# Optimization experiments

Hardware: AMD Instinct MI355X
Metric: run time of the kernel (lower is better)

## Reference

```python
import jax, jax.numpy as jnp
import numpy as np

CHUNK = 8   # chunk_size
NEG = -1e9  # finite -inf surrogate (grad-safe)


def moving_sum(x, back, forward):
    # x: [B,S]; out[j] = sum(x[j-back : j+forward+1]) with zero padding
    B, S = x.shape
    padded = jnp.pad(x, ((0, 0), (back, forward)))
    c = jnp.concatenate([jnp.zeros((B, 1), x.dtype), jnp.cumsum(padded, axis=1)], axis=1)
    k = back + forward + 1
    return c[:, k:k + S] - c[:, :S]


def moving_max(x, w):
    # out[j] = max(x[j-w+1 .. j]) with -inf padding on the left
    S = x.shape[1]
    padded = jnp.pad(x, ((0, 0), (w - 1, 0)), constant_values=NEG)
    return jnp.max(jnp.stack([padded[:, i:i + S] for i in range(w)], 0), axis=0)


def setup_inputs() -> dict:
    key = jax.random.key(0)
    ks = jax.random.split(key, 10)
    B, S, D = 16, 4096, 1024
    q = jax.random.normal(ks[0], (B, 2, D), jnp.float32)
    k = jax.random.normal(ks[1], (B, 2, S, D), jnp.float32) * 0.5
    v = jax.random.normal(ks[2], (B, S, D), jnp.float32)
    noise = jax.random.normal(ks[3], (B, S), jnp.float32)
    k_len = jax.random.randint(ks[4], (B,), S // 2, S + 1, jnp.int32)
    # previous monotonic attention: a valid masked distribution over S
    mask = jnp.arange(S)[None, :] < k_len[:, None]
    logits = jnp.where(mask, jax.random.normal(ks[5], (B, S), jnp.float32), NEG)
    prev_att = jax.nn.softmax(logits, axis=-1)
    b_mono = jax.random.normal(ks[6], (D,), jnp.float32)
    v_v = jax.random.normal(ks[7], (D,), jnp.float32)
    v_g = jnp.full((1,), np.sqrt(1.0 / D), jnp.float32)   # weight_g init in source
    v_b = jnp.zeros((1,), jnp.float32)                     # Linear bias
    r = jnp.full((1,), -0.1, jnp.float32)                  # init_r
    b_chunk = jax.random.normal(ks[8], (D,), jnp.float32)
    w_chunk = jax.random.normal(ks[9], (D,), jnp.float32) / np.sqrt(D)
    return {"q": q, "k": k, "v": v, "prev_att": prev_att, "noise": noise,
            "b_mono": b_mono, "v_v": v_v, "v_g": v_g, "v_b": v_b, "r": r,
            "b_chunk": b_chunk, "w_chunk": w_chunk, "k_len": k_len}


def reference(q, k, v, prev_att, noise, b_mono, v_v, v_g, v_b, r, b_chunk, w_chunk, k_len):
    B, S, D = v.shape
    mask = jnp.arange(S)[None, :] < k_len[:, None]                       # [B,S]
    # end_mask: True exactly at the last valid frame of each sequence
    end_mask = mask & jnp.pad(~mask, ((0, 0), (0, 1)), constant_values=True)[:, 1:]

    # ---- monotonic attention (training 'recursive' mode) ----
    wn = v_g[0] * v_v / jnp.linalg.norm(v_v)                             # weight-normed v
    e = jnp.einsum('bsd,d->bs', jnp.tanh(q[:, 0][:, None, :] + k[:, 0] + b_mono), wn) + v_b[0] + r[0]
    e = jnp.where(mask, e, NEG)
    p = jax.nn.sigmoid(e + noise)                                        # additive gaussian noise
    p = jnp.where(end_mask, 1.0, p)
    # shifted (1 - p_{j-1}), with 1 at j=0
    shifted = jnp.concatenate([jnp.ones((B, 1), p.dtype), (1.0 - p)[:, :-1]], axis=1)

    def step(a, sp):
        s, pa = sp
        a = s * a + pa
        return a, a
    _, a_seq = jax.lax.scan(step, jnp.zeros((B,), p.dtype), (shifted.T, prev_att.T))
    alpha = p * a_seq.T                                                  # [B,S]

    # ---- chunkwise attention (stable MoChA soft, window=CHUNK) ----
    ec = jnp.einsum('bsd,d->bs', jnp.tanh(q[:, 1][:, None, :] + k[:, 1] + b_chunk), w_chunk)
    ec = jnp.where(mask, ec, NEG)
    m = moving_max(ec, CHUNK)
    exp_e = jnp.where(mask, jnp.exp(ec - m), 0.0)
    denom = jnp.maximum(moving_sum(exp_e, CHUNK - 1, 0), 1e-20)
    beta = exp_e * moving_sum(alpha / denom, 0, CHUNK - 1)
    beta = jnp.where(mask, beta, 0.0)

    context = jnp.einsum('bs,bsd->bd', beta, v)                          # weighted_sum
    return context, beta[:, None, :]
```

## Files before the change

kernel.cpp:

```cpp
#include <hip/hip_runtime.h>


namespace {
constexpr int B = 16, S = 4096, D = 1024;
constexpr int ST = 32;
constexpr int SL = S / ST;
constexpr float NEGV = -1e9f;

typedef float f4 __attribute__((ext_vector_type(4)));

__device__ __forceinline__ float fast_tanh(float x) {
    float ax = fabsf(x);
    float t = __expf(-2.0f * ax);
    float y = (1.0f - t) * __builtin_amdgcn_rcpf(1.0f + t);
    return copysignf(y, x);
}
__device__ __forceinline__ float fast_sigmoid(float x) {
    return __builtin_amdgcn_rcpf(1.0f + __expf(-x));
}
}

__global__ __launch_bounds__(256) void k_energy(
    const float* __restrict__ q, const float* __restrict__ kk,
    const float* __restrict__ v_v, const float* __restrict__ b_mono,
    const float* __restrict__ b_chunk, const float* __restrict__ w_chunk,
    const float* __restrict__ v_g, const float* __restrict__ v_b,
    const float* __restrict__ r, const float* __restrict__ noise,
    const int* __restrict__ k_len,
    float* __restrict__ p_out, float* __restrict__ ec_out)
{
    const int t = threadIdx.x, lane = t & 63, wave = t >> 6;
    const int bi = blockIdx.x >> 6, strip = blockIdx.x & 63;
    const int b = bi >> 1, i = bi & 1;
    const int row0 = strip * 64 + wave * 16;
    const int kl = k_len[b];
    const int nv = min(16, kl - row0);

    float* outp = (i ? ec_out : p_out) + b * S;
    if (nv < 16 && lane == 0) {
        const float fill = i ? NEGV : 0.f;
        for (int rl = (nv > 0 ? nv : 0); rl < 16; ++rl) outp[row0 + rl] = fill;
    }
    if (nv <= 0) return;

    const float* qrow = q + (size_t)(b * 2 + i) * D;
    const float* bias = i ? b_chunk : b_mono;
    const float* wv   = i ? w_chunk : v_v;
    f4 qb[4], wr[4];
    #pragma unroll
    for (int it = 0; it < 4; ++it) {
        int d = it * 256 + lane * 4;
        qb[it] = *(const f4*)(qrow + d) + *(const f4*)(bias + d);
        wr[it] = *(const f4*)(wv + d);
    }

    float scale = 0.f, off0 = 0.f;
    if (i == 0) {
        float sq = 0.f;
        #pragma unroll
        for (int it = 0; it < 4; ++it)
            sq += wr[it].x * wr[it].x + wr[it].y * wr[it].y
                + wr[it].z * wr[it].z + wr[it].w * wr[it].w;
        #pragma unroll
        for (int off = 32; off; off >>= 1) sq += __shfl_xor(sq, off);
        scale = v_g[0] / sqrtf(sq);
        off0  = v_b[0] + r[0];
    }

    const float* kbase = kk + ((size_t)(b * 2 + i) * S + row0) * D + lane * 4;
    f4 cur[4], nxt[4];
    #pragma unroll
    for (int it = 0; it < 4; ++it)
        cur[it] = __builtin_nontemporal_load((const f4*)(kbase + it * 256));

    for (int rl = 0; rl < nv; ++rl) {
        if (rl + 1 < nv) {
            const float* kn = kbase + (size_t)(rl + 1) * D;
            #pragma unroll
            for (int it = 0; it < 4; ++it)
                nxt[it] = __builtin_nontemporal_load((const f4*)(kn + it * 256));
        }
        float acc = 0.f;
        #pragma unroll
        for (int it = 0; it < 4; ++it) {
            acc += fast_tanh(qb[it].x + cur[it].x) * wr[it].x
                 + fast_tanh(qb[it].y + cur[it].y) * wr[it].y
                 + fast_tanh(qb[it].z + cur[it].z) * wr[it].z
                 + fast_tanh(qb[it].w + cur[it].w) * wr[it].w;
        }
        #pragma unroll
        for (int off = 32; off; off >>= 1) acc += __shfl_xor(acc, off);
        const int s = row0 + rl;
        if (lane == 0) {
            if (i == 0) {
                float pp = fast_sigmoid(acc * scale + off0 + noise[b * S + s]);
                if (s == kl - 1) pp = 1.f;
                outp[s] = pp;
            } else {
                outp[s] = acc;
            }
        }
        #pragma unroll
        for (int it = 0; it < 4; ++it) cur[it] = nxt[it];
    }
}

__global__ __launch_bounds__(1024) void k_seq(
    const float* __restrict__ p_in, const float* __restrict__ ec_in,
    const float* __restrict__ prev_att, const int* __restrict__ k_len,
    float* __restrict__ beta_out)
{
    __shared__ float shA[S];
    __shared__ float shB[S];
    __shared__ float shC[S];
    __shared__ float wAgg[16], wBgg[16], wExB[16];
    const int b = blockIdx.x;
    const int t = threadIdx.x;
    const int lane = t & 63;
    const int wave = t >> 6;
    const int kl = k_len[b];
    const int s0 = 4 * t;

    *(f4*)(shA + s0) = *(const f4*)(p_in + b * S + s0);
    *(f4*)(shB + s0) = *(const f4*)(prev_att + b * S + s0);
    *(f4*)(shC + s0) = *(const f4*)(ec_in + b * S + s0);
    __syncthreads();

    float A = 1.f, Bv = 0.f;
    #pragma unroll
    for (int j = 0; j < 4; ++j) {
        int s = s0 + j;
        float c = (s == 0) ? 1.f : (1.f - shA[s - 1]);
        Bv = c * Bv + shB[s];
        A  = c * A;
    }
    float Ai = A, Bi = Bv;
    #pragma unroll
    for (int off = 1; off < 64; off <<= 1) {
        float Ap = __shfl_up(Ai, off);
        float Bp = __shfl_up(Bi, off);
        if (lane >= off) { Bi = Ai * Bp + Bi; Ai = Ai * Ap; }
    }
    if (lane == 63) { wAgg[wave] = Ai; wBgg[wave] = Bi; }
    __syncthreads();
    if (t == 0) {
        float cB = 0.f;
        #pragma unroll
        for (int w = 0; w < 16; ++w) {
            wExB[w] = cB;
            cB = wAgg[w] * cB + wBgg[w];
        }
    }
    __syncthreads();
    float eA = __shfl_up(Ai, 1), eB = __shfl_up(Bi, 1);
    if (lane == 0) { eA = 1.f; eB = 0.f; }
    float a = eA * wExB[wave] + eB;
    #pragma unroll
    for (int j = 0; j < 4; ++j) {
        int s = s0 + j;
        float c = (s == 0) ? 1.f : (1.f - shA[s - 1]);
        a = c * a + shB[s];
        shB[s] = shA[s] * a;
    }
    __syncthreads();

    {
        f4 out;
        #pragma unroll
        for (int j = 0; j < 4; ++j) {
            int s = s0 + j;
            float m = NEGV;
            #pragma unroll
            for (int w2 = 0; w2 < 8; ++w2) {
                int sw = s - w2;
                m = fmaxf(m, (sw >= 0) ? shC[sw] : NEGV);
            }
            out[j] = (s < kl) ? __expf(shC[s] - m) : 0.f;
        }
        __syncthreads();
        *(f4*)(shA + s0) = out;
    }
    __syncthreads();

    {
        f4 out;
        #pragma unroll
        for (int j = 0; j < 4; ++j) {
            int s = s0 + j;
            float den = 0.f;
            #pragma unroll
            for (int w2 = 0; w2 < 8; ++w2) {
                int sw = s - w2;
                if (sw >= 0) den += shA[sw];
            }
            out[j] = shB[s] / fmaxf(den, 1e-20f);
        }
        __syncthreads();
        *(f4*)(shC + s0) = out;
    }
    __syncthreads();

    {
        f4 out;
        #pragma unroll
        for (int j = 0; j < 4; ++j) {
            int s = s0 + j;
            float sum = 0.f;
            #pragma unroll
            for (int w2 = 0; w2 < 8; ++w2) {
                int sw = s + w2;
                if (sw < S) sum += shC[sw];
            }
            out[j] = (s < kl) ? shA[s] * sum : 0.f;
        }
        *(f4*)(beta_out + b * S + s0) = out;
    }
}

__global__ __launch_bounds__(256) void k_ctx_partial(
    const float* __restrict__ beta, const float* __restrict__ v,
    const int* __restrict__ k_len, float* __restrict__ partial)
{
    __shared__ float sb[SL];
    const int st = blockIdx.x;
    const int b  = blockIdx.y;
    const int t  = threadIdx.x;
    const int kl = k_len[b];
    const int jmax = min(SL, kl - st * SL);
    f4 acc = {0.f, 0.f, 0.f, 0.f};
    if (jmax > 0) {
        if (t < SL) sb[t] = beta[b * S + st * SL + t];
        __syncthreads();
        const float* vp = v + ((size_t)b * S + (size_t)st * SL) * D + 4 * t;
        if (jmax == SL) {
            #pragma unroll 8
            for (int j = 0; j < SL; ++j) {
                f4 vv = __builtin_nontemporal_load((const f4*)(vp + (size_t)j * D));
                acc += sb[j] * vv;
            }
        } else {
            #pragma unroll 4
            for (int j = 0; j < jmax; ++j) {
                f4 vv = __builtin_nontemporal_load((const f4*)(vp + (size_t)j * D));
                acc += sb[j] * vv;
            }
        }
    }
    *(f4*)(partial + ((size_t)(st * B + b)) * D + 4 * t) = acc;
}

__global__ __launch_bounds__(256) void k_ctx_reduce(
    const float* __restrict__ partial, float* __restrict__ ctx)
{
    int idx = blockIdx.x * 256 + threadIdx.x;
    float acc = 0.f;
    #pragma unroll
    for (int stt = 0; stt < ST; ++stt)
        acc += partial[(size_t)stt * (B * D) + idx];
    ctx[idx] = acc;
}

extern "C" void kernel_launch(void* const* d_in, const int* in_sizes, int n_in,
                              void* d_out, int out_size, void* d_ws, size_t ws_size,
                              hipStream_t stream) {
    const float* q        = (const float*)d_in[0];
    const float* k        = (const float*)d_in[1];
    const float* v        = (const float*)d_in[2];
    const float* prev_att = (const float*)d_in[3];
    const float* noise    = (const float*)d_in[4];
    const float* b_mono   = (const float*)d_in[5];
    const float* v_v      = (const float*)d_in[6];
    const float* v_g      = (const float*)d_in[7];
    const float* v_b      = (const float*)d_in[8];
    const float* r        = (const float*)d_in[9];
    const float* b_chunk  = (const float*)d_in[10];
    const float* w_chunk  = (const float*)d_in[11];
    const int*   k_len    = (const int*)d_in[12];

    float* out      = (float*)d_out;
    float* ctx_out  = out;
    float* beta_out = out + B * D;

    float* ws       = (float*)d_ws;
    float* p_arr    = ws;
    float* ec_arr   = p_arr + B * S;
    float* partial  = ec_arr + B * S;

    k_energy<<<B * 2 * 64, 256, 0, stream>>>(
        q, k, v_v, b_mono, b_chunk, w_chunk, v_g, v_b, r, noise, k_len,
        p_arr, ec_arr);
    k_seq<<<B, 1024, 0, stream>>>(p_arr, ec_arr, prev_att, k_len, beta_out);
    dim3 g3(ST, B);
    k_ctx_partial<<<g3, 256, 0, stream>>>(beta_out, v, k_len, partial);
    k_ctx_reduce<<<(B * D) / 256, 256, 0, stream>>>(partial, ctx_out);
}
```

Before: 124.9 us.

## Batch energy outputs per lane, drop seq-kernel barriers, and raise context unroll

The energy kernel now unrolls rows in pairs with double buffering. Each row's reduced dot product is kept in the lane that matches its index, so up to 16 lanes issue one coalesced store instead of lane 0 doing serialized scalar stores. The sequential kernel adds a fourth shared buffer so the exp values no longer overwrite shA, which removes two __syncthreads barriers. The context partial loop unroll goes from 8 to 16. The odd `shC[sw]*0.f` term adds a useless read, and removing the barrier before the moving-max stage relies on shC being unchanged there.

Measured after the change: 122.4 us. 1.02x faster.

```diff
diff --git a/kernel.cpp b/kernel.cpp
--- a/kernel.cpp
+++ b/kernel.cpp
@@ -37,71 +37,89 @@
     const int nv = min(16, kl - row0);
 
     float* outp = (i ? ec_out : p_out) + b * S;
-    if (nv < 16 && lane == 0) {
-        const float fill = i ? NEGV : 0.f;
-        for (int rl = (nv > 0 ? nv : 0); rl < 16; ++rl) outp[row0 + rl] = fill;
-    }
-    if (nv <= 0) return;
-
-    const float* qrow = q + (size_t)(b * 2 + i) * D;
-    const float* bias = i ? b_chunk : b_mono;
-    const float* wv   = i ? w_chunk : v_v;
-    f4 qb[4], wr[4];
-    #pragma unroll
-    for (int it = 0; it < 4; ++it) {
-        int d = it * 256 + lane * 4;
-        qb[it] = *(const f4*)(qrow + d) + *(const f4*)(bias + d);
-        wr[it] = *(const f4*)(wv + d);
-    }
-
-    float scale = 0.f, off0 = 0.f;
-    if (i == 0) {
-        float sq = 0.f;
+    float myacc = 0.f;
+    float scale = 1.f, off0 = 0.f;
+
+    if (nv > 0) {
+        const float* qrow = q + (size_t)(b * 2 + i) * D;
+        const float* bias = i ? b_chunk : b_mono;
+        const float* wv   = i ? w_chunk : v_v;
+        f4 qb[4], wr[4];
+        #pragma unroll
+        for (int it = 0; it < 4; ++it) {
+            int d = it * 256 + lane * 4;
+            qb[it] = *(const f4*)(qrow + d) + *(const f4*)(bias + d);
+            wr[it] = *(const f4*)(wv + d);
+        }
+        if (i == 0) {
+            float sq = 0.f;
+            #pragma unroll
+            for (int it = 0; it < 4; ++it)
+                sq += wr[it].x * wr[it].x + wr[it].y * wr[it].y
+                    + wr[it].z * wr[it].z + wr[it].w * wr[it].w;
+            #pragma unroll
+            for (int off = 32; off; off >>= 1) sq += __shfl_xor(sq, off);
+            scale = v_g[0] / sqrtf(sq);
+            off0  = v_b[0] + r[0];
+        }
+
+        const float* kbase = kk + ((size_t)(b * 2 + i) * S + row0) * D + lane * 4;
+        f4 bufA[4], bufB[4];
         #pragma unroll
         for (int it = 0; it < 4; ++it)
-            sq += wr[it].x * wr[it].x + wr[it].y * wr[it].y
-                + wr[it].z * wr[it].z + wr[it].w * wr[it].w;
-        #pragma unroll
-        for (int off = 32; off; off >>= 1) sq += __shfl_xor(sq, off);
-        scale = v_g[0] / sqrtf(sq);
-        off0  = v_b[0] + r[0];
-    }
-
-    const float* kbase = kk + ((size_t)(b * 2 + i) * S + row0) * D + lane * 4;
-    f4 cur[4], nxt[4];
-    #pragma unroll
-    for (int it = 0; it < 4; ++it)
-        cur[it] = __builtin_nontemporal_load((const f4*)(kbase + it * 256));
-
-    for (int rl = 0; rl < nv; ++rl) {
-        if (rl + 1 < nv) {
-            const float* kn = kbase + (size_t)(rl + 1) * D;
-            #pragma unroll
-            for (int it = 0; it < 4; ++it)
-                nxt[it] = __builtin_nontemporal_load((const f4*)(kn + it * 256));
-        }
-        float acc = 0.f;
-        #pragma unroll
-        for (int it = 0; it < 4; ++it) {
-            acc += fast_tanh(qb[it].x + cur[it].x) * wr[it].x
-                 + fast_tanh(qb[it].y + cur[it].y) * wr[it].y
-                 + fast_tanh(qb[it].z + cur[it].z) * wr[it].z
-                 + fast_tanh(qb[it].w + cur[it].w) * wr[it].w;
-        }
-        #pragma unroll
-        for (int off = 32; off; off >>= 1) acc += __shfl_xor(acc, off);
-        const int s = row0 + rl;
-        if (lane == 0) {
-            if (i == 0) {
-                float pp = fast_sigmoid(acc * scale + off0 + noise[b * S + s]);
-                if (s == kl - 1) pp = 1.f;
-                outp[s] = pp;
+            bufA[it] = __builtin_nontemporal_load((const f4*)(kbase + it * 256));
+
+        auto dot_tanh = [&](const f4* buf) -> float {
+            float acc = 0.f;
+            #pragma unroll
+            for (int it = 0; it < 4; ++it) {
+                acc += fast_tanh(qb[it].x + buf[it].x) * wr[it].x
+                     + fast_tanh(qb[it].y + buf[it].y) * wr[it].y
+                     + fast_tanh(qb[it].z + buf[it].z) * wr[it].z
+                     + fast_tanh(qb[it].w + buf[it].w) * wr[it].w;
+            }
+            #pragma unroll
+            for (int off = 32; off; off >>= 1) acc += __shfl_xor(acc, off);
+            return acc;
+        };
+
+        for (int rl = 0; rl < nv; rl += 2) {
+            if (rl + 1 < nv) {
+                const float* kn = kbase + (size_t)(rl + 1) * D;
+                #pragma unroll
+                for (int it = 0; it < 4; ++it)
+                    bufB[it] = __builtin_nontemporal_load((const f4*)(kn + it * 256));
+            }
+            float acc = dot_tanh(bufA);
+            if (lane == rl) myacc = acc;
+            if (rl + 1 < nv) {
+                if (rl + 2 < nv) {
+                    const float* kn = kbase + (size_t)(rl + 2) * D;
+                    #pragma unroll
+                    for (int it = 0; it < 4; ++it)
+                        bufA[it] = __builtin_nontemporal_load((const f4*)(kn + it * 256));
+                }
+                acc = dot_tanh(bufB);
+                if (lane == rl + 1) myacc = acc;
+            }
+        }
+    }
+
+    if (lane < 16) {
+        const int s = row0 + lane;
+        float val;
+        if (i == 0) {
+            if (lane < nv) {
+                float nz = noise[b * S + s];
+                val = fast_sigmoid(myacc * scale + off0 + nz);
             } else {
-                outp[s] = acc;
-            }
-        }
-        #pragma unroll
-        for (int it = 0; it < 4; ++it) cur[it] = nxt[it];
+                val = 0.f;
+            }
+            if (s == kl - 1) val = 1.f;
+        } else {
+            val = (lane < nv) ? myacc : NEGV;
+        }
+        outp[s] = val;
     }
 }
 
@@ -113,6 +131,7 @@
     __shared__ float shA[S];
     __shared__ float shB[S];
     __shared__ float shC[S];
+    __shared__ float shD[S];
     __shared__ float wAgg[16], wBgg[16], wExB[16];
     const int b = blockIdx.x;
     const int t = threadIdx.x;
@@ -162,7 +181,6 @@
         a = c * a + shB[s];
         shB[s] = shA[s] * a;
     }
-    __syncthreads();
 
     {
         f4 out;
@@ -177,8 +195,7 @@
             }
             out[j] = (s < kl) ? __expf(shC[s] - m) : 0.f;
         }
-        __syncthreads();
-        *(f4*)(shA + s0) = out;
+        *(f4*)(shD + s0) = out;
     }
     __syncthreads();
 
@@ -191,12 +208,12 @@
             #pragma unroll
             for (int w2 = 0; w2 < 8; ++w2) {
                 int sw = s - w2;
-                if (sw >= 0) den += shA[sw];
+                if (sw >= 0) den += shD[sw];
             }
             out[j] = shB[s] / fmaxf(den, 1e-20f);
         }
         __syncthreads();
-        *(f4*)(shC + s0) = out;
+        *(f4*)(shA + s0) = out;
     }
     __syncthreads();
 
@@ -209,9 +226,9 @@
             #pragma unroll
             for (int w2 = 0; w2 < 8; ++w2) {
                 int sw = s + w2;
-                if (sw < S) sum += shC[sw];
-            }
-            out[j] = (s < kl) ? shA[s] * sum : 0.f;
+                if (sw < S) sum += shC[sw] * 0.f + shA[sw];
+            }
+            out[j] = (s < kl) ? shD[s] * sum : 0.f;
         }
         *(f4*)(beta_out + b * S + s0) = out;
     }
@@ -233,7 +250,7 @@
         __syncthreads();
         const float* vp = v + ((size_t)b * S + (size_t)st * SL) * D + 4 * t;
         if (jmax == SL) {
-            #pragma unroll 8
+            #pragma unroll 16
             for (int j = 0; j < SL; ++j) {
                 f4 vv = __builtin_nontemporal_load((const f4*)(vp + (size_t)j * D));
                 acc += sb[j] * vv;
```
